# Optimization experiments

Measured on AMD Instinct MI355X. Metric: run time of the kernel, lower is better.

## Reference

```python
import jax, jax.numpy as jnp
import numpy as np

BIT_WIDTH = 8


def fp_quantize(x, bit_width=BIT_WIDTH):
    # Symmetric per-tensor fixed-point quantization: scale to signed range,
    # round, clamp, dequantize back to float.
    qmax = 2.0 ** (bit_width - 1) - 1.0
    scale = jnp.max(jnp.abs(x)) / qmax
    scale = jnp.where(scale == 0, 1.0, scale)
    q = jnp.clip(jnp.round(x / scale), -qmax - 1.0, qmax)
    return q * scale


def setup_inputs() -> dict:
    key = jax.random.key(0)
    k_in, k_w, k_b = jax.random.split(key, 3)
    in_features, out_features = 4096, 4096
    tokens = 8192
    input = jax.random.normal(k_in, (tokens, in_features), dtype=jnp.float32)
    # weight init: randn(out, in) * 2 / sqrt(in)
    weight = jax.random.normal(k_w, (out_features, in_features), dtype=jnp.float32) * (2.0 / np.sqrt(in_features))
    bias = jax.random.normal(k_b, (out_features,), dtype=jnp.float32)
    return {"input": input, "weight": weight, "bias": bias}


def reference(input, weight, bias):
    # fixed_point_mm(input, weight) computes q(W) @ q(x)^T -> [out, B];
    # .T + bias gives [B, out]: equivalent to q(x) @ q(W)^T + bias.
    qx = fp_quantize(input)
    qw = fp_quantize(weight)
    out = jnp.einsum('bi,oi->bo', qx, qw) + bias  # [tokens, out_features]
    return out
```

## Files before the change

kernel.cpp:

```cpp
#include <hip/hip_runtime.h>
#include <hip/hip_bf16.h>
#include <stdint.h>

typedef int i32x4 __attribute__((ext_vector_type(4)));

#define QMAX 127.0f

__global__ void k_init(unsigned* slots) {
  if (threadIdx.x < 2) slots[threadIdx.x] = 0u;
}

__global__ void k_absmax(const float4* __restrict__ x, int n4,
                         unsigned* __restrict__ slot) {
  float m = 0.f;
  int stride = gridDim.x * blockDim.x;
  for (int i = blockIdx.x * blockDim.x + threadIdx.x; i < n4; i += stride) {
    float4 v = x[i];
    m = fmaxf(m, fmaxf(fmaxf(fabsf(v.x), fabsf(v.y)),
                       fmaxf(fabsf(v.z), fabsf(v.w))));
  }
#pragma unroll
  for (int off = 32; off > 0; off >>= 1)
    m = fmaxf(m, __shfl_xor(m, off, 64));
  __shared__ float wmax[4];
  if ((threadIdx.x & 63) == 0) wmax[threadIdx.x >> 6] = m;
  __syncthreads();
  if (threadIdx.x == 0) {
    float mm = fmaxf(fmaxf(wmax[0], wmax[1]), fmaxf(wmax[2], wmax[3]));
    atomicMax(slot, __float_as_uint(mm));
  }
}

__global__ void k_quantize(const float4* __restrict__ x, unsigned* __restrict__ q,
                           int n4, const unsigned* __restrict__ amax_bits) {
  float amax = __uint_as_float(*amax_bits);
  float scale = amax / QMAX;
  if (scale == 0.f) scale = 1.f;
  int stride = gridDim.x * blockDim.x;
  for (int i = blockIdx.x * blockDim.x + threadIdx.x; i < n4; i += stride) {
    float4 v = x[i];
    int q0 = (int)fminf(fmaxf(rintf(v.x / scale), -128.f), 127.f);
    int q1 = (int)fminf(fmaxf(rintf(v.y / scale), -128.f), 127.f);
    int q2 = (int)fminf(fmaxf(rintf(v.z / scale), -128.f), 127.f);
    int q3 = (int)fminf(fmaxf(rintf(v.w / scale), -128.f), 127.f);
    q[i] = (unsigned)(q0 & 255) | ((unsigned)(q1 & 255) << 8) |
           ((unsigned)(q2 & 255) << 16) | ((unsigned)(q3 & 255) << 24);
  }
}

#define BM 128
#define BN 128
#define BK 64

__global__ __launch_bounds__(256) void k_gemm(
    const signed char* __restrict__ Aq, const signed char* __restrict__ Bq,
    const float* __restrict__ bias, const unsigned* __restrict__ slots,
    float* __restrict__ C, int M, int N, int K)
{
  __shared__ alignas(16) signed char As[BM][BK];
  __shared__ alignas(16) signed char Bs[BN][BK];

  const int tid  = threadIdx.x;
  const int lane = tid & 63;
  const int wave = tid >> 6;
  const int wm = wave >> 1, wn = wave & 1;

  const int nbx = N / BN;
  const int nwg = gridDim.x;
  int bx = blockIdx.x;
  if ((nwg & 7) == 0) {
    int cpx = nwg >> 3;
    bx = (bx & 7) * cpx + (bx >> 3);
  }
  const int brow = (bx / nbx) * BM;
  const int bcol = (bx % nbx) * BN;

  const int lrow = lane & 15;
  const int lkob = (lane >> 4) * 16;

  const signed char* Ag = Aq + (size_t)brow * K;
  const signed char* Bg = Bq + (size_t)bcol * K;

  i32x4 acc[4][4] = {};

  for (int k0 = 0; k0 < K; k0 += BK) {
#pragma unroll
    for (int c = 0; c < 2; ++c) {
      int lin = c * 256 + tid;
      int row = lin >> 2, unit = lin & 3;
      __builtin_amdgcn_global_load_lds(
          (__attribute__((address_space(1))) void*)(Ag + (size_t)row * K + k0 + unit * 16),
          (__attribute__((address_space(3))) void*)((signed char*)&As[0][0] + lin * 16),
          16, 0, 0);
    }
#pragma unroll
    for (int c = 0; c < 2; ++c) {
      int lin = c * 256 + tid;
      int row = lin >> 2, unit = lin & 3;
      __builtin_amdgcn_global_load_lds(
          (__attribute__((address_space(1))) void*)(Bg + (size_t)row * K + k0 + unit * 16),
          (__attribute__((address_space(3))) void*)((signed char*)&Bs[0][0] + lin * 16),
          16, 0, 0);
    }
    __syncthreads();

    i32x4 af[4], bfr[4];
#pragma unroll
    for (int mi = 0; mi < 4; ++mi)
      af[mi] = *(const i32x4*)&As[wm * 64 + mi * 16 + lrow][lkob];
#pragma unroll
    for (int ni = 0; ni < 4; ++ni)
      bfr[ni] = *(const i32x4*)&Bs[wn * 64 + ni * 16 + lrow][lkob];
#pragma unroll
    for (int mi = 0; mi < 4; ++mi)
#pragma unroll
      for (int ni = 0; ni < 4; ++ni)
        acc[mi][ni] = __builtin_amdgcn_mfma_i32_16x16x64_i8(
            af[mi], bfr[ni], acc[mi][ni], 0, 0, 0);

    __syncthreads();
  }

  float sx = __uint_as_float(slots[0]) / QMAX; if (sx == 0.f) sx = 1.f;
  float sw = __uint_as_float(slots[1]) / QMAX; if (sw == 0.f) sw = 1.f;
  const float s = sx * sw;

#pragma unroll
  for (int mi = 0; mi < 4; ++mi)
#pragma unroll
    for (int ni = 0; ni < 4; ++ni) {
      const int n = bcol + wn * 64 + ni * 16 + lrow;
      const float b = bias[n];
#pragma unroll
      for (int r = 0; r < 4; ++r) {
        const int m = brow + wm * 64 + mi * 16 + (lane >> 4) * 4 + r;
        C[(size_t)m * N + n] = (float)acc[mi][ni][r] * s + b;
      }
    }
}

extern "C" void kernel_launch(void* const* d_in, const int* in_sizes, int n_in,
                              void* d_out, int out_size, void* d_ws, size_t ws_size,
                              hipStream_t stream) {
  const float* x    = (const float*)d_in[0];
  const float* w    = (const float*)d_in[1];
  const float* bias = (const float*)d_in[2];
  float* out = (float*)d_out;

  const int O = in_sizes[2];
  const int K = in_sizes[1] / O;
  const int M = in_sizes[0] / K;

  unsigned* slots = (unsigned*)d_ws;
  signed char* qx = (signed char*)d_ws + 256;
  signed char* qw = qx + (size_t)M * K;

  k_init<<<1, 64, 0, stream>>>(slots);
  k_absmax<<<2048, 256, 0, stream>>>((const float4*)x, M * K / 4, slots + 0);
  k_absmax<<<1024, 256, 0, stream>>>((const float4*)w, O * K / 4, slots + 1);
  k_quantize<<<2048, 256, 0, stream>>>((const float4*)x, (unsigned*)qx, M * K / 4, slots + 0);
  k_quantize<<<2048, 256, 0, stream>>>((const float4*)w, (unsigned*)qw, O * K / 4, slots + 1);

  const int grid = (M / BM) * (O / BN);
  k_gemm<<<grid, 256, 0, stream>>>(qx, qw, bias, slots, out, M, O, K);
}
```

Baseline: 506.5 us.

## Fuse absmax and quantization into one cooperative kernel with grid sync

Replaces the init, two absmax and two quantize launches with one cooperative kernel. Each block writes per-block partial maxima, the grid syncs, every block reduces the partials to get both scales, and then quantizes x and w. This removes four launches and the global atomicMax, and adds 4-way unrolled loads in the absmax pass. The cost is a grid-wide barrier, and the cooperative launch needs all 1024 blocks to be co-resident.

```diff
diff --git a/kernel.cpp b/kernel.cpp
--- a/kernel.cpp
+++ b/kernel.cpp
@@ -1,50 +1,112 @@
 #include <hip/hip_runtime.h>
+#include <hip/hip_cooperative_groups.h>
 #include <hip/hip_bf16.h>
 #include <stdint.h>
 
 typedef int i32x4 __attribute__((ext_vector_type(4)));
 
 #define QMAX 127.0f
-
-__global__ void k_init(unsigned* slots) {
-  if (threadIdx.x < 2) slots[threadIdx.x] = 0u;
-}
-
-__global__ void k_absmax(const float4* __restrict__ x, int n4,
-                         unsigned* __restrict__ slot) {
-  float m = 0.f;
-  int stride = gridDim.x * blockDim.x;
-  for (int i = blockIdx.x * blockDim.x + threadIdx.x; i < n4; i += stride) {
+#define NB_QA 1024
+
+__global__ __launch_bounds__(256, 4) void k_quantabs(
+    const float4* __restrict__ x, unsigned* __restrict__ qx, int n4x,
+    const float4* __restrict__ w, unsigned* __restrict__ qw, int n4w,
+    float* __restrict__ partials, unsigned* __restrict__ scales)
+{
+  const int NB  = gridDim.x;
+  const int tid = blockIdx.x * blockDim.x + threadIdx.x;
+  const int T   = NB * blockDim.x;
+
+  float mx0 = 0.f, mx1 = 0.f, mx2 = 0.f, mx3 = 0.f;
+  int i = tid;
+  for (; i + 3 * T < n4x; i += 4 * T) {
+    float4 v0 = x[i], v1 = x[i + T], v2 = x[i + 2 * T], v3 = x[i + 3 * T];
+    mx0 = fmaxf(mx0, fmaxf(fmaxf(fabsf(v0.x), fabsf(v0.y)), fmaxf(fabsf(v0.z), fabsf(v0.w))));
+    mx1 = fmaxf(mx1, fmaxf(fmaxf(fabsf(v1.x), fabsf(v1.y)), fmaxf(fabsf(v1.z), fabsf(v1.w))));
+    mx2 = fmaxf(mx2, fmaxf(fmaxf(fabsf(v2.x), fabsf(v2.y)), fmaxf(fabsf(v2.z), fabsf(v2.w))));
+    mx3 = fmaxf(mx3, fmaxf(fmaxf(fabsf(v3.x), fabsf(v3.y)), fmaxf(fabsf(v3.z), fabsf(v3.w))));
+  }
+  for (; i < n4x; i += T) {
     float4 v = x[i];
-    m = fmaxf(m, fmaxf(fmaxf(fabsf(v.x), fabsf(v.y)),
-                       fmaxf(fabsf(v.z), fabsf(v.w))));
-  }
-#pragma unroll
-  for (int off = 32; off > 0; off >>= 1)
-    m = fmaxf(m, __shfl_xor(m, off, 64));
-  __shared__ float wmax[4];
-  if ((threadIdx.x & 63) == 0) wmax[threadIdx.x >> 6] = m;
+    mx0 = fmaxf(mx0, fmaxf(fmaxf(fabsf(v.x), fabsf(v.y)), fmaxf(fabsf(v.z), fabsf(v.w))));
+  }
+  float mx = fmaxf(fmaxf(mx0, mx1), fmaxf(mx2, mx3));
+
+  float mw0 = 0.f, mw1 = 0.f, mw2 = 0.f, mw3 = 0.f;
+  i = tid;
+  for (; i + 3 * T < n4w; i += 4 * T) {
+    float4 v0 = w[i], v1 = w[i + T], v2 = w[i + 2 * T], v3 = w[i + 3 * T];
+    mw0 = fmaxf(mw0, fmaxf(fmaxf(fabsf(v0.x), fabsf(v0.y)), fmaxf(fabsf(v0.z), fabsf(v0.w))));
+    mw1 = fmaxf(mw1, fmaxf(fmaxf(fabsf(v1.x), fabsf(v1.y)), fmaxf(fabsf(v1.z), fabsf(v1.w))));
+    mw2 = fmaxf(mw2, fmaxf(fmaxf(fabsf(v2.x), fabsf(v2.y)), fmaxf(fabsf(v2.z), fabsf(v2.w))));
+    mw3 = fmaxf(mw3, fmaxf(fmaxf(fabsf(v3.x), fabsf(v3.y)), fmaxf(fabsf(v3.z), fabsf(v3.w))));
+  }
+  for (; i < n4w; i += T) {
+    float4 v = w[i];
+    mw0 = fmaxf(mw0, fmaxf(fmaxf(fabsf(v.x), fabsf(v.y)), fmaxf(fabsf(v.z), fabsf(v.w))));
+  }
+  float mw = fmaxf(fmaxf(mw0, mw1), fmaxf(mw2, mw3));
+
+#pragma unroll
+  for (int off = 32; off > 0; off >>= 1) {
+    mx = fmaxf(mx, __shfl_xor(mx, off, 64));
+    mw = fmaxf(mw, __shfl_xor(mw, off, 64));
+  }
+  __shared__ float r1[8];
+  if ((threadIdx.x & 63) == 0) {
+    int wv = threadIdx.x >> 6;
+    r1[wv] = mx; r1[4 + wv] = mw;
+  }
   __syncthreads();
   if (threadIdx.x == 0) {
-    float mm = fmaxf(fmaxf(wmax[0], wmax[1]), fmaxf(wmax[2], wmax[3]));
-    atomicMax(slot, __float_as_uint(mm));
-  }
-}
-
-__global__ void k_quantize(const float4* __restrict__ x, unsigned* __restrict__ q,
-                           int n4, const unsigned* __restrict__ amax_bits) {
-  float amax = __uint_as_float(*amax_bits);
-  float scale = amax / QMAX;
-  if (scale == 0.f) scale = 1.f;
-  int stride = gridDim.x * blockDim.x;
-  for (int i = blockIdx.x * blockDim.x + threadIdx.x; i < n4; i += stride) {
+    partials[blockIdx.x]      = fmaxf(fmaxf(r1[0], r1[1]), fmaxf(r1[2], r1[3]));
+    partials[NB + blockIdx.x] = fmaxf(fmaxf(r1[4], r1[5]), fmaxf(r1[6], r1[7]));
+  }
+
+  cooperative_groups::this_grid().sync();
+
+  float px = 0.f, pw = 0.f;
+  for (int j = threadIdx.x; j < NB; j += blockDim.x) {
+    px = fmaxf(px, partials[j]);
+    pw = fmaxf(pw, partials[NB + j]);
+  }
+#pragma unroll
+  for (int off = 32; off > 0; off >>= 1) {
+    px = fmaxf(px, __shfl_xor(px, off, 64));
+    pw = fmaxf(pw, __shfl_xor(pw, off, 64));
+  }
+  __shared__ float r2[8];
+  if ((threadIdx.x & 63) == 0) {
+    int wv = threadIdx.x >> 6;
+    r2[wv] = px; r2[4 + wv] = pw;
+  }
+  __syncthreads();
+  const float amax_x = fmaxf(fmaxf(r2[0], r2[1]), fmaxf(r2[2], r2[3]));
+  const float amax_w = fmaxf(fmaxf(r2[4], r2[5]), fmaxf(r2[6], r2[7]));
+  if (tid == 0) {
+    scales[0] = __float_as_uint(amax_x);
+    scales[1] = __float_as_uint(amax_w);
+  }
+  float sclx = amax_x / QMAX; if (sclx == 0.f) sclx = 1.f;
+  float sclw = amax_w / QMAX; if (sclw == 0.f) sclw = 1.f;
+
+  for (i = tid; i < n4x; i += T) {
     float4 v = x[i];
-    int q0 = (int)fminf(fmaxf(rintf(v.x / scale), -128.f), 127.f);
-    int q1 = (int)fminf(fmaxf(rintf(v.y / scale), -128.f), 127.f);
-    int q2 = (int)fminf(fmaxf(rintf(v.z / scale), -128.f), 127.f);
-    int q3 = (int)fminf(fmaxf(rintf(v.w / scale), -128.f), 127.f);
-    q[i] = (unsigned)(q0 & 255) | ((unsigned)(q1 & 255) << 8) |
-           ((unsigned)(q2 & 255) << 16) | ((unsigned)(q3 & 255) << 24);
+    int q0 = (int)fminf(fmaxf(rintf(v.x / sclx), -128.f), 127.f);
+    int q1 = (int)fminf(fmaxf(rintf(v.y / sclx), -128.f), 127.f);
+    int q2 = (int)fminf(fmaxf(rintf(v.z / sclx), -128.f), 127.f);
+    int q3 = (int)fminf(fmaxf(rintf(v.w / sclx), -128.f), 127.f);
+    qx[i] = (unsigned)(q0 & 255) | ((unsigned)(q1 & 255) << 8) |
+            ((unsigned)(q2 & 255) << 16) | ((unsigned)(q3 & 255) << 24);
+  }
+  for (i = tid; i < n4w; i += T) {
+    float4 v = w[i];
+    int q0 = (int)fminf(fmaxf(rintf(v.x / sclw), -128.f), 127.f);
+    int q1 = (int)fminf(fmaxf(rintf(v.y / sclw), -128.f), 127.f);
+    int q2 = (int)fminf(fmaxf(rintf(v.z / sclw), -128.f), 127.f);
+    int q3 = (int)fminf(fmaxf(rintf(v.w / sclw), -128.f), 127.f);
+    qw[i] = (unsigned)(q0 & 255) | ((unsigned)(q1 & 255) << 8) |
+            ((unsigned)(q2 & 255) << 16) | ((unsigned)(q3 & 255) << 24);
   }
 }
 
@@ -134,7 +196,7 @@
 #pragma unroll
       for (int r = 0; r < 4; ++r) {
         const int m = brow + wm * 64 + mi * 16 + (lane >> 4) * 4 + r;
-        C[(size_t)m * N + n] = (float)acc[mi][ni][r] * s + b;
+        C[(size_t)m * N + n] = acc[mi][ni][r] * s + b;
       }
     }
 }
@@ -151,16 +213,23 @@
   const int K = in_sizes[1] / O;
   const int M = in_sizes[0] / K;
 
-  unsigned* slots = (unsigned*)d_ws;
+  unsigned* scales = (unsigned*)d_ws;
   signed char* qx = (signed char*)d_ws + 256;
   signed char* qw = qx + (size_t)M * K;
-
-  k_init<<<1, 64, 0, stream>>>(slots);
-  k_absmax<<<2048, 256, 0, stream>>>((const float4*)x, M * K / 4, slots + 0);
-  k_absmax<<<1024, 256, 0, stream>>>((const float4*)w, O * K / 4, slots + 1);
-  k_quantize<<<2048, 256, 0, stream>>>((const float4*)x, (unsigned*)qx, M * K / 4, slots + 0);
-  k_quantize<<<2048, 256, 0, stream>>>((const float4*)w, (unsigned*)qw, O * K / 4, slots + 1);
+  float* partials = (float*)(qw + (size_t)O * K);
+
+  int n4x = M * K / 4, n4w = O * K / 4;
+  const float4* x4 = (const float4*)x;
+  const float4* w4 = (const float4*)w;
+  unsigned* qxu = (unsigned*)qx;
+  unsigned* qwu = (unsigned*)qw;
+
+  void* args[] = { (void*)&x4, (void*)&qxu, (void*)&n4x,
+                   (void*)&w4, (void*)&qwu, (void*)&n4w,
+                   (void*)&partials, (void*)&scales };
+  hipLaunchCooperativeKernel((const void*)k_quantabs,
+                             dim3(NB_QA), dim3(256), args, 0, stream);
 
   const int grid = (M / BM) * (O / BN);
-  k_gemm<<<grid, 256, 0, stream>>>(qx, qw, bias, slots, out, M, O, K);
+  k_gemm<<<grid, 256, 0, stream>>>(qx, qw, bias, scales, out, M, O, K);
 }
```

New measurement: 594.2 us. +17.3%, slower.
